# Optimization experiments

Hardware: AMD Instinct MI355X
Metric: run time of the kernel (lower is better)

The kernel has to match this reference:

```python
import itertools
import jax, jax.numpy as jnp
import numpy as np

B, N, C, O = 8, 32, 64, 64
PERMS = list(itertools.permutations((1, 2, 3)))  # build_idx_3_permutations order


def _lin(k, fan_in, out, lead=()):
    # torch nn.Linear default init: U(-1/sqrt(fan_in), 1/sqrt(fan_in)) for W and b
    kw, kb = jax.random.split(k)
    bound = 1.0 / float(np.sqrt(fan_in))
    W = jax.random.uniform(kw, lead + (fan_in, out), minval=-bound, maxval=bound, dtype=jnp.float32)
    b = jax.random.uniform(kb, lead + (out,), minval=-bound, maxval=bound, dtype=jnp.float32)
    return W, b


def setup_inputs() -> dict:
    key = jax.random.key(0)
    ks = jax.random.split(key, 8)
    x = jax.random.normal(ks[0], (B, N, N, N, C), dtype=jnp.float32)
    W33, b33 = _lin(ks[1], 6 * C, O)            # three_to_three linear
    W22, b22 = _lin(ks[2], 12 * C, O, (3,))     # two_to_two (a2 cat transpose), 3 diagonal planes
    W12, b12 = _lin(ks[3], 10 * C, O, (3,))     # one_to_two
    W12t, b12t = _lin(ks[4], 10 * C, O, (3,))   # one_to_two_t
    W02, b02 = _lin(ks[5], 5 * C, O, (3,))      # zero_to_two
    W11, b11 = _lin(ks[6], 10 * C, O)           # one_to_one (in_node_channels = 0)
    W01, b01 = _lin(ks[7], 5 * C, O)            # zero_to_one
    return dict(x=x, W33=W33, b33=b33, W22=W22, b22=b22, W12=W12, b12=b12,
                W12t=W12t, b12t=b12t, W02=W02, b02=b02, W11=W11, b11=b11,
                W01=W01, b01=b01)


def _contractions(x):
    """All second/first/zeroth-order mean contractions of x: [B,n,n,n,C]."""
    s1, s2, s3 = x.mean(1), x.mean(2), x.mean(3)                      # [B,n,n,C]
    # diagonals arranged as [B, other_axis, diag_axis, C]
    d12 = jnp.moveaxis(jnp.diagonal(x, axis1=1, axis2=2), -1, 2)      # [B,n3,diag,C]
    d13 = jnp.moveaxis(jnp.diagonal(x, axis1=1, axis2=3), -1, 2)      # [B,n2,diag,C]
    d23 = jnp.moveaxis(jnp.diagonal(x, axis1=2, axis2=3), -1, 2)      # [B,n1,diag,C]
    a2 = jnp.concatenate([s1, s2, s3, d12, d13, d23], axis=-1)        # [B,n,n,6C]
    tdiag = jnp.moveaxis(jnp.diagonal(d23, axis1=1, axis2=2), -1, 1)  # [B,n,C] triple diagonal x[b,i,i,i]
    a1 = jnp.concatenate([
        x.mean((1, 2)), x.mean((1, 3)), x.mean((2, 3)),               # double sums
        d12.mean(1), d12.mean(2), d13.mean(1), d13.mean(2),           # diag sums
        d23.mean(1), d23.mean(2),
        tdiag], axis=-1)                                              # [B,n,10C]
    a0 = jnp.concatenate([
        x.mean((1, 2, 3)),                                            # triple sum
        d12.mean((1, 2)), d13.mean((1, 2)), d23.mean((1, 2)),         # diag-sum-sum
        tdiag.mean(1)], axis=-1)                                      # [B,5C]
    return a2, a1, a0


def reference(x, W33, b33, W22, b22, W12, b12, W12t, b12t, W02, b02, W11, b11, W01, b01):
    n = x.shape[1]
    a2, a1, a0 = _contractions(x)
    # third-order mix: concat all 6 spatial permutations, then linear 6C -> O
    allp = jnp.concatenate([jnp.transpose(x, (0,) + p + (4,)) for p in PERMS], axis=-1)
    T = allp @ W33 + b33                                              # [B,n,n,n,O]
    # second-order mixes for the 3 diagonal planes
    a2wt = jnp.concatenate([a2, jnp.swapaxes(a2, 1, 2)], axis=-1)     # [B,n,n,12C]
    slices = []
    for i in range(3):
        m = a2wt @ W22[i] + b22[i]
        m = m + (a1 @ W12[i] + b12[i])[:, :, None, :]
        m = m + (a1 @ W12t[i] + b12t[i])[:, None, :, :]
        m = m + (a0 @ W02[i] + b02[i])[:, None, None, :]
        slices.append(m)                                              # [B,n(other),n(diag),O]
    # first-order (core-diagonal) mix
    mdiag = a1 @ W11 + b11 + (a0 @ W01 + b01)[:, None, :]             # [B,n,O]
    # _expand_mix: accumulate slices onto diagonal planes of T (diagonal_free=False)
    idx = jnp.arange(n)
    # plane (1,2): T[b,d,d,t] += slices[0][b,t,d]
    T = T.at[:, idx, idx].add(jnp.swapaxes(slices[0], 1, 2))
    # plane (1,3): T[b,d,t,d] += slices[1][b,t,d]
    Tsw = jnp.swapaxes(T, 2, 3)
    Tsw = Tsw.at[:, idx, idx].add(jnp.swapaxes(slices[1], 1, 2))
    T = jnp.swapaxes(Tsw, 2, 3)
    # plane (2,3): T[b,t,d,d] += slices[2][b,t,d]
    T = T.at[:, :, idx, idx].add(slices[2])
    # triple diagonal: T[b,d,d,d] += mdiag[b,d]
    T = T.at[:, idx, idx, idx].add(mdiag)
    return T
```

## Files before the change

kernel.cpp:

```cpp
#include <hip/hip_runtime.h>

#define NBATCH 8
#define NN 32
#define NC 64
#define NO 64
#define C6 384
#define C10 640
#define C12 768
#define C5 320

typedef __attribute__((ext_vector_type(8))) short short8;
typedef __attribute__((ext_vector_type(4))) float float4v;

static constexpr int OFF_ABF = 0;
static constexpr int OFF_A1  = 1572864;
static constexpr int OFF_A0  = 1736704;
static constexpr int OFF_R1  = 1739264;
static constexpr int OFF_R1T = 1788416;
static constexpr int OFF_R0  = 1837568;
static constexpr int OFF_MD  = 1839104;
static constexpr int OFF_WB  = 1855488;
static constexpr int OFF_WB2 = 1867776;

__device__ __forceinline__ unsigned short f2bf(float f) {
    union { float f; unsigned u; } x{f};
    unsigned r = x.u + 0x7fffu + ((x.u >> 16) & 1u);
    return (unsigned short)(r >> 16);
}

__device__ __forceinline__ void store_bf4(unsigned short* p, float4v v) {
    ushort4 w;
    w.x = f2bf(v.x); w.y = f2bf(v.y); w.z = f2bf(v.z); w.w = f2bf(v.w);
    *(ushort4*)p = w;
}

__device__ __forceinline__ float4v bf4(const unsigned short* p) {
    ushort4 u = *(const ushort4*)(p);
    float4v r;
    r.x = __uint_as_float((unsigned)u.x << 16);
    r.y = __uint_as_float((unsigned)u.y << 16);
    r.z = __uint_as_float((unsigned)u.z << 16);
    r.w = __uint_as_float((unsigned)u.w << 16);
    return r;
}

__global__ __launch_bounds__(256) void k_prepw(const float* __restrict__ W33,
                                               const float* __restrict__ W22,
                                               float* __restrict__ ws) {
    int id = blockIdx.x * 256 + threadIdx.x;
    if (id < 3072) {
        int lane = id & 63;
        int ks = (id >> 6) % 12;
        int nt = (id >> 6) / 12;
        int n = nt * 16 + (lane & 15);
        int k0 = ks * 32 + (lane >> 4) * 8;
        unsigned short* dst = (unsigned short*)(ws + OFF_WB) +
                              (size_t)((nt * 12 + ks) * 64 + lane) * 8;
#pragma unroll
        for (int jj = 0; jj < 8; ++jj) dst[jj] = f2bf(W33[(k0 + jj) * 64 + n]);
    } else if (id < 21504) {
        int q = id - 3072;
        int lane = q & 63;
        int ks = (q >> 6) % 24;
        int r = (q >> 6) / 24;
        int nt = r & 3;
        int i = r >> 2;
        int n = nt * 16 + (lane & 15);
        int k0 = ks * 32 + (lane >> 4) * 8;
        const float* W = W22 + (size_t)i * C12 * NO;
        unsigned short* dst = (unsigned short*)(ws + OFF_WB2) +
                              (size_t)(((i * 4 + nt) * 24 + ks) * 64 + lane) * 8;
#pragma unroll
        for (int jj = 0; jj < 8; ++jj) dst[jj] = f2bf(W[(k0 + jj) * 64 + n]);
    }
}

__global__ __launch_bounds__(256) void k_contract2(const float* __restrict__ x,
                                                   float* __restrict__ ws) {
    int id = blockIdx.x * 256 + threadIdx.x;
    int c4 = id & 15;
    int v = (id >> 4) & 31;
    int u = (id >> 9) & 31;
    int b = id >> 14;
    int bc = c4 * 4;
    const float* xb = x + (size_t)b * 2097152;

    float4v s1 = {0.f, 0.f, 0.f, 0.f}, s2 = s1, s3 = s1;
    {
        const float* p = xb + u * 2048 + v * 64 + bc;
        for (int i = 0; i < 32; ++i) s1 += *(const float4v*)(p + i * 65536);
    }
    {
        const float* p = xb + u * 65536 + v * 64 + bc;
        for (int j = 0; j < 32; ++j) s2 += *(const float4v*)(p + j * 2048);
    }
    {
        const float* p = xb + u * 65536 + v * 2048 + bc;
        for (int k = 0; k < 32; ++k) s3 += *(const float4v*)(p + k * 64);
    }
    float4v d12 = *(const float4v*)(xb + v * 65536 + v * 2048 + u * 64 + bc);
    float4v d13 = *(const float4v*)(xb + v * 65536 + u * 2048 + v * 64 + bc);
    float4v d23 = *(const float4v*)(xb + u * 65536 + v * 2048 + v * 64 + bc);

    const float inv = 1.0f / 32.0f;
    unsigned short* a2 = (unsigned short*)(ws + OFF_ABF) +
                         (size_t)((b * 32 + u) * 32 + v) * C6 + bc;
    store_bf4(a2 + 0 * 64, s1 * inv);
    store_bf4(a2 + 1 * 64, s2 * inv);
    store_bf4(a2 + 2 * 64, s3 * inv);
    store_bf4(a2 + 3 * 64, d12);
    store_bf4(a2 + 4 * 64, d13);
    store_bf4(a2 + 5 * 64, d23);
}

__global__ __launch_bounds__(256) void k_contract1(const float* __restrict__ x,
                                                   float* __restrict__ ws) {
    __shared__ float4v red[16][148];
    int blk = blockIdx.x;
    int b = blk >> 5;
    int t = blk & 31;
    int tid = threadIdx.x;
    int c4 = tid & 15;
    int q = tid >> 4;
    int bc = c4 * 4;
    const unsigned short* a2 = (const unsigned short*)(ws + OFF_ABF) +
                               (size_t)b * 32 * 32 * C6;

    float4v pu0 = {0.f, 0.f, 0.f, 0.f};
    float4v pu3 = pu0, pu4 = pu0, pu5 = pu0;
    float4v pv0 = pu0, pv1 = pu0, pv3 = pu0, pv4 = pu0, pv5 = pu0;
#pragma unroll
    for (int s = 0; s < 2; ++s) {
        int u = q * 2 + s;
        const unsigned short* rU = a2 + (size_t)(u * 32 + t) * C6 + bc;
        const unsigned short* rV = a2 + (size_t)(t * 32 + u) * C6 + bc;
        pu0 += bf4(rU + 0);
        pu3 += bf4(rU + 192);
        pu4 += bf4(rU + 256);
        pu5 += bf4(rU + 320);
        pv0 += bf4(rV + 0);
        pv1 += bf4(rV + 64);
        pv3 += bf4(rV + 192);
        pv4 += bf4(rV + 256);
        pv5 += bf4(rV + 320);
    }
    red[q][0 * 16 + c4] = pu0;
    red[q][1 * 16 + c4] = pv0;
    red[q][2 * 16 + c4] = pv1;
    red[q][3 * 16 + c4] = pu3;
    red[q][4 * 16 + c4] = pv3;
    red[q][5 * 16 + c4] = pu4;
    red[q][6 * 16 + c4] = pv4;
    red[q][7 * 16 + c4] = pu5;
    red[q][8 * 16 + c4] = pv5;
    __syncthreads();

    const float inv = 1.0f / 32.0f;
    float* a1 = ws + OFF_A1 + ((size_t)b * 32 + t) * C10;
    float* a0 = ws + OFF_A0 + (size_t)b * C5;
    if (tid < 144) {
        int ch = tid >> 4;
        int cc = tid & 15;
        float4v s = {0.f, 0.f, 0.f, 0.f};
#pragma unroll
        for (int qq = 0; qq < 16; ++qq) s += red[qq][ch * 16 + cc];
        s *= inv;
        *(float4v*)(a1 + ch * 64 + cc * 4) = s;
        int aidx = (ch == 0) ? 0 : (ch == 3) ? 1 : (ch == 5) ? 2 : (ch == 7) ? 3 : -1;
        if (aidx >= 0) {
#pragma unroll
            for (int e = 0; e < 4; ++e)
                atomicAdd(a0 + aidx * 64 + cc * 4 + e, s[e] * inv);
        }
    } else if (tid < 160) {
        int cc = tid - 144;
        float4v td = *(const float4v*)(x + (((size_t)b * 32 + t) * 32 + t) * 2048 +
                                       t * 64 + cc * 4);
        *(float4v*)(a1 + 9 * 64 + cc * 4) = td;
#pragma unroll
        for (int e = 0; e < 4; ++e)
            atomicAdd(a0 + 4 * 64 + cc * 4 + e, td[e] * inv);
    }
}

__global__ __launch_bounds__(256) void k_rowmix(
    const float* __restrict__ W12, const float* __restrict__ b12,
    const float* __restrict__ W12t, const float* __restrict__ b12t,
    const float* __restrict__ W02, const float* __restrict__ b02,
    const float* __restrict__ W11, const float* __restrict__ b11,
    const float* __restrict__ W01, const float* __restrict__ b01,
    float* __restrict__ ws) {
    int id = blockIdx.x * 256 + threadIdx.x;
    if (id < 98304) {
        bool second = id >= 49152;
        int q = second ? id - 49152 : id;
        int o = q & 63;
        int t = (q >> 6) & 31;
        int b = (q >> 11) & 7;
        int i = q >> 14;
        const float* W = (second ? W12t : W12) + (size_t)i * C10 * NO;
        const float* bb = (second ? b12t : b12) + i * NO;
        const float* a1 = ws + OFF_A1 + ((size_t)b * 32 + t) * C10;
        float acc = bb[o];
        for (int m = 0; m < C10; ++m) acc += a1[m] * W[m * NO + o];
        ws[(second ? OFF_R1T : OFF_R1) + (((size_t)i * 8 + b) * 32 + t) * NO + o] = acc;
    } else if (id < 114688) {
        int q = id - 98304;
        int o = q & 63;
        int t = (q >> 6) & 31;
        int b = q >> 11;
        const float* a1 = ws + OFF_A1 + ((size_t)b * 32 + t) * C10;
        const float* a0 = ws + OFF_A0 + (size_t)b * C5;
        float acc = b11[o] + b01[o];
        for (int m = 0; m < C10; ++m) acc += a1[m] * W11[m * NO + o];
        for (int m = 0; m < C5; ++m) acc += a0[m] * W01[m * NO + o];
        ws[OFF_MD + ((size_t)b * 32 + t) * NO + o] = acc;
    } else if (id < 116224) {
        int q = id - 114688;
        int o = q & 63;
        int b = (q >> 6) & 7;
        int i = q >> 9;
        const float* a0 = ws + OFF_A0 + (size_t)b * C5;
        float acc = b02[i * NO + o];
        for (int m = 0; m < C5; ++m) acc += a0[m] * W02[(size_t)i * C5 * NO + m * NO + o];
        ws[OFF_R0 + ((size_t)i * 8 + b) * NO + o] = acc;
    }
}

__global__ __launch_bounds__(256) void k_main(const float* __restrict__ x,
                                              const float* __restrict__ ws,
                                              const float* __restrict__ b33,
                                              float* __restrict__ T) {
    __shared__ __align__(16) unsigned short As[32 * 392];
    int tid = threadIdx.x;
    const unsigned short* WB = (const unsigned short*)(ws + OFF_WB);

    int wv = tid >> 6;
    int lane = tid & 63;
    int m_tile = wv & 1;
    int n_pair = wv >> 1;
    int colq = lane & 15;
    int quad = lane >> 4;

    short8 bfr[2][12];
#pragma unroll
    for (int np = 0; np < 2; ++np) {
        int nt = n_pair * 2 + np;
#pragma unroll
        for (int ks = 0; ks < 12; ++ks)
            bfr[np][ks] = *(const short8*)(WB + (size_t)((nt * 12 + ks) * 64 + lane) * 8);
    }
    float bb0 = b33[(n_pair * 2 + 0) * 16 + colq];
    float bb1 = b33[(n_pair * 2 + 1) * 16 + colq];

    int k0 = wv * 8;
    int c = colq * 4;
    int mrow = m_tile * 16 + colq;
    const unsigned short* Arow = &As[mrow * 392 + quad * 8];

    int tbase = (blockIdx.x & 7) * 1024 + (blockIdx.x >> 3) * 4;
#pragma unroll 1
    for (int r = 0; r < 4; ++r) {
        int tile = tbase + r;
        int b = tile >> 10;
        int i = (tile >> 5) & 31;
        int j = tile & 31;
        const float* xb = x + (size_t)b * 2097152;

#pragma unroll
        for (int half = 0; half < 2; ++half) {
            int k = k0 + quad + half * 4;
            float4v v0 = *(const float4v*)(xb + i * 65536 + j * 2048 + k * 64 + c);
            float4v v1 = *(const float4v*)(xb + i * 65536 + k * 2048 + j * 64 + c);
            float4v v2 = *(const float4v*)(xb + j * 65536 + i * 2048 + k * 64 + c);
            float4v v3 = *(const float4v*)(xb + k * 65536 + i * 2048 + j * 64 + c);
            float4v v4 = *(const float4v*)(xb + j * 65536 + k * 2048 + i * 64 + c);
            float4v v5 = *(const float4v*)(xb + k * 65536 + j * 2048 + i * 64 + c);
            unsigned short* dst = &As[k * 392 + c];
            store_bf4(dst + 0 * 64, v0);
            store_bf4(dst + 1 * 64, v1);
            store_bf4(dst + 2 * 64, v2);
            store_bf4(dst + 3 * 64, v3);
            store_bf4(dst + 4 * 64, v4);
            store_bf4(dst + 5 * 64, v5);
        }
        __syncthreads();

        float4v acc0 = {0.f, 0.f, 0.f, 0.f};
        float4v acc1 = {0.f, 0.f, 0.f, 0.f};
#pragma unroll
        for (int ks = 0; ks < 12; ++ks) {
            short8 a = *(const short8*)(Arow + ks * 32);
            acc0 = __builtin_amdgcn_mfma_f32_16x16x32_bf16(a, bfr[0][ks], acc0, 0, 0, 0);
            acc1 = __builtin_amdgcn_mfma_f32_16x16x32_bf16(a, bfr[1][ks], acc1, 0, 0, 0);
        }

        float* Tb = T + (size_t)tile * 2048;
#pragma unroll
        for (int rr = 0; rr < 4; ++rr) {
            int m = m_tile * 16 + quad * 4 + rr;
            int o0 = (n_pair * 2 + 0) * 16 + colq;
            int o1 = (n_pair * 2 + 1) * 16 + colq;
            __builtin_nontemporal_store(acc0[rr] + bb0, &Tb[m * 64 + o0]);
            __builtin_nontemporal_store(acc1[rr] + bb1, &Tb[m * 64 + o1]);
        }
        __syncthreads();
    }
}

__global__ __launch_bounds__(512) void k_slices(const float* __restrict__ b22,
                                                float* __restrict__ T,
                                                const float* __restrict__ ws) {
    __shared__ __align__(16) unsigned short As[32 * 776];
    int blk = blockIdx.x;
    int b = blk >> 5;
    int t = blk & 31;
    int tid = threadIdx.x;
    const unsigned short* abf = (const unsigned short*)(ws + OFF_ABF);
    const unsigned short* WB2 = (const unsigned short*)(ws + OFF_WB2);

    for (int l = tid; l < 3072; l += 512) {
        int d = l / 96;
        int m8 = l - d * 96;
        const unsigned short* src = (m8 < 48)
            ? abf + (size_t)(((b * 32 + t) * 32 + d) * C6) + m8 * 8
            : abf + (size_t)(((b * 32 + d) * 32 + t) * C6) + (m8 - 48) * 8;
        *(short8*)&As[d * 776 + m8 * 8] = *(const short8*)src;
    }
    __syncthreads();

    int wv = tid >> 6;
    int lane = tid & 63;
    int mt = wv & 1;
    int nt = wv >> 1;
    float4v zero = {0.f, 0.f, 0.f, 0.f};
    float4v acc[3] = {zero, zero, zero};
    const unsigned short* Arow = &As[(mt * 16 + (lane & 15)) * 776 + (lane >> 4) * 8];
#pragma unroll
    for (int ks = 0; ks < 24; ++ks) {
        short8 a = *(const short8*)(Arow + ks * 32);
#pragma unroll
        for (int i = 0; i < 3; ++i) {
            short8 bf = *(const short8*)(WB2 + (size_t)(((i * 4 + nt) * 24 + ks) * 64 + lane) * 8);
            acc[i] = __builtin_amdgcn_mfma_f32_16x16x32_bf16(a, bf, acc[i], 0, 0, 0);
        }
    }

    int colq = lane & 15;
    int quad = lane >> 4;
    float* Tb = T + (size_t)b * 2097152;
    int o = nt * 16 + colq;
    float base0 = b22[0 * 64 + o] + ws[OFF_R1 + ((size_t)(0 * 8 + b) * 32 + t) * 64 + o]
                + ws[OFF_R0 + (size_t)(0 * 8 + b) * 64 + o];
    float base1 = b22[1 * 64 + o] + ws[OFF_R1 + ((size_t)(1 * 8 + b) * 32 + t) * 64 + o]
                + ws[OFF_R0 + (size_t)(1 * 8 + b) * 64 + o];
    float base2 = b22[2 * 64 + o] + ws[OFF_R1 + ((size_t)(2 * 8 + b) * 32 + t) * 64 + o]
                + ws[OFF_R0 + (size_t)(2 * 8 + b) * 64 + o];
#pragma unroll
    for (int r = 0; r < 4; ++r) {
        int d = mt * 16 + quad * 4 + r;
        float s0 = acc[0][r] + base0 + ws[OFF_R1T + ((size_t)(0 * 8 + b) * 32 + d) * 64 + o];
        float s1 = acc[1][r] + base1 + ws[OFF_R1T + ((size_t)(1 * 8 + b) * 32 + d) * 64 + o];
        float s2 = acc[2][r] + base2 + ws[OFF_R1T + ((size_t)(2 * 8 + b) * 32 + d) * 64 + o];
        if (d != t) {
            Tb[d * 65536 + d * 2048 + t * 64 + o] += s0;
            Tb[d * 65536 + t * 2048 + d * 64 + o] += s1;
            Tb[t * 65536 + d * 2048 + d * 64 + o] += s2;
        } else {
            float md = ws[OFF_MD + ((size_t)b * 32 + d) * 64 + o];
            Tb[d * 65536 + d * 2048 + d * 64 + o] += s0 + s1 + s2 + md;
        }
    }
}

extern "C" void kernel_launch(void* const* d_in, const int* in_sizes, int n_in,
                              void* d_out, int out_size, void* d_ws, size_t ws_size,
                              hipStream_t stream) {
    const float* x    = (const float*)d_in[0];
    const float* W33  = (const float*)d_in[1];
    const float* b33  = (const float*)d_in[2];
    const float* W22  = (const float*)d_in[3];
    const float* b22  = (const float*)d_in[4];
    const float* W12  = (const float*)d_in[5];
    const float* b12  = (const float*)d_in[6];
    const float* W12t = (const float*)d_in[7];
    const float* b12t = (const float*)d_in[8];
    const float* W02  = (const float*)d_in[9];
    const float* b02  = (const float*)d_in[10];
    const float* W11  = (const float*)d_in[11];
    const float* b11  = (const float*)d_in[12];
    const float* W01  = (const float*)d_in[13];
    const float* b01  = (const float*)d_in[14];
    float* T  = (float*)d_out;
    float* ws = (float*)d_ws;

    hipLaunchKernelGGL(k_prepw, dim3(84), dim3(256), 0, stream, W33, W22, ws);
    hipLaunchKernelGGL(k_contract2, dim3(512), dim3(256), 0, stream, x, ws);
    hipMemsetAsync(ws + OFF_A0, 0, (size_t)NBATCH * C5 * sizeof(float), stream);
    hipLaunchKernelGGL(k_contract1, dim3(256), dim3(256), 0, stream, x, ws);
    hipLaunchKernelGGL(k_rowmix, dim3(454), dim3(256), 0, stream,
                       W12, b12, W12t, b12t, W02, b02, W11, b11, W01, b01, ws);
    hipLaunchKernelGGL(k_main, dim3(2048), dim3(256), 0, stream, x, ws, b33, T);
    hipLaunchKernelGGL(k_slices, dim3(256), dim3(512), 0, stream, b22, T, ws);
}
```

Baseline: 250.4 us.

## Fuse weight prep with contraction and fold row mixes into neighbouring kernels

Merges the weight bf16 repacking kernel with the second-order contraction kernel into one launch, computes the W12/W12t row mixes inside k_contract1 from a shared-memory copy of a1, and computes the diagonal and zeroth-order mixes inside k_slices. This removes two kernel launches and the separate k_rowmix pass with its global round trips. In exchange, k_contract1 and k_slices each do extra serial dot-product work per block, which could lengthen their critical path.

New measurement: 274.4 us. +9.6%, slower.

```diff
diff --git a/kernel.cpp b/kernel.cpp
--- a/kernel.cpp
+++ b/kernel.cpp
@@ -44,40 +44,40 @@
     return r;
 }
 
-__global__ __launch_bounds__(256) void k_prepw(const float* __restrict__ W33,
+__global__ __launch_bounds__(256) void k_prep2(const float* __restrict__ W33,
                                                const float* __restrict__ W22,
+                                               const float* __restrict__ x,
                                                float* __restrict__ ws) {
-    int id = blockIdx.x * 256 + threadIdx.x;
-    if (id < 3072) {
-        int lane = id & 63;
-        int ks = (id >> 6) % 12;
-        int nt = (id >> 6) / 12;
-        int n = nt * 16 + (lane & 15);
-        int k0 = ks * 32 + (lane >> 4) * 8;
-        unsigned short* dst = (unsigned short*)(ws + OFF_WB) +
-                              (size_t)((nt * 12 + ks) * 64 + lane) * 8;
-#pragma unroll
-        for (int jj = 0; jj < 8; ++jj) dst[jj] = f2bf(W33[(k0 + jj) * 64 + n]);
-    } else if (id < 21504) {
-        int q = id - 3072;
-        int lane = q & 63;
-        int ks = (q >> 6) % 24;
-        int r = (q >> 6) / 24;
-        int nt = r & 3;
-        int i = r >> 2;
-        int n = nt * 16 + (lane & 15);
-        int k0 = ks * 32 + (lane >> 4) * 8;
-        const float* W = W22 + (size_t)i * C12 * NO;
-        unsigned short* dst = (unsigned short*)(ws + OFF_WB2) +
-                              (size_t)(((i * 4 + nt) * 24 + ks) * 64 + lane) * 8;
-#pragma unroll
-        for (int jj = 0; jj < 8; ++jj) dst[jj] = f2bf(W[(k0 + jj) * 64 + n]);
-    }
-}
-
-__global__ __launch_bounds__(256) void k_contract2(const float* __restrict__ x,
-                                                   float* __restrict__ ws) {
-    int id = blockIdx.x * 256 + threadIdx.x;
+    if (blockIdx.x < 84) {
+        int id = blockIdx.x * 256 + threadIdx.x;
+        if (id < 3072) {
+            int lane = id & 63;
+            int ks = (id >> 6) % 12;
+            int nt = (id >> 6) / 12;
+            int n = nt * 16 + (lane & 15);
+            int k0 = ks * 32 + (lane >> 4) * 8;
+            unsigned short* dst = (unsigned short*)(ws + OFF_WB) +
+                                  (size_t)((nt * 12 + ks) * 64 + lane) * 8;
+#pragma unroll
+            for (int jj = 0; jj < 8; ++jj) dst[jj] = f2bf(W33[(k0 + jj) * 64 + n]);
+        } else if (id < 21504) {
+            int q = id - 3072;
+            int lane = q & 63;
+            int ks = (q >> 6) % 24;
+            int r = (q >> 6) / 24;
+            int nt = r & 3;
+            int i = r >> 2;
+            int n = nt * 16 + (lane & 15);
+            int k0 = ks * 32 + (lane >> 4) * 8;
+            const float* W = W22 + (size_t)i * C12 * NO;
+            unsigned short* dst = (unsigned short*)(ws + OFF_WB2) +
+                                  (size_t)(((i * 4 + nt) * 24 + ks) * 64 + lane) * 8;
+#pragma unroll
+            for (int jj = 0; jj < 8; ++jj) dst[jj] = f2bf(W[(k0 + jj) * 64 + n]);
+        }
+        return;
+    }
+    int id = (blockIdx.x - 84) * 256 + threadIdx.x;
     int c4 = id & 15;
     int v = (id >> 4) & 31;
     int u = (id >> 9) & 31;
@@ -113,9 +113,13 @@
     store_bf4(a2 + 5 * 64, d23);
 }
 
-__global__ __launch_bounds__(256) void k_contract1(const float* __restrict__ x,
-                                                   float* __restrict__ ws) {
+__global__ __launch_bounds__(256) void k_contract1(
+    const float* __restrict__ x,
+    const float* __restrict__ W12, const float* __restrict__ b12,
+    const float* __restrict__ W12t, const float* __restrict__ b12t,
+    float* __restrict__ ws) {
     __shared__ float4v red[16][148];
+    __shared__ float a1buf[C10];
     int blk = blockIdx.x;
     int b = blk >> 5;
     int t = blk & 31;
@@ -166,6 +170,8 @@
         for (int qq = 0; qq < 16; ++qq) s += red[qq][ch * 16 + cc];
         s *= inv;
         *(float4v*)(a1 + ch * 64 + cc * 4) = s;
+#pragma unroll
+        for (int e = 0; e < 4; ++e) a1buf[ch * 64 + cc * 4 + e] = s[e];
         int aidx = (ch == 0) ? 0 : (ch == 3) ? 1 : (ch == 5) ? 2 : (ch == 7) ? 3 : -1;
         if (aidx >= 0) {
 #pragma unroll
@@ -178,52 +184,32 @@
                                        t * 64 + cc * 4);
         *(float4v*)(a1 + 9 * 64 + cc * 4) = td;
 #pragma unroll
-        for (int e = 0; e < 4; ++e)
+        for (int e = 0; e < 4; ++e) {
+            a1buf[9 * 64 + cc * 4 + e] = td[e];
             atomicAdd(a0 + 4 * 64 + cc * 4 + e, td[e] * inv);
-    }
-}
-
-__global__ __launch_bounds__(256) void k_rowmix(
-    const float* __restrict__ W12, const float* __restrict__ b12,
-    const float* __restrict__ W12t, const float* __restrict__ b12t,
-    const float* __restrict__ W02, const float* __restrict__ b02,
-    const float* __restrict__ W11, const float* __restrict__ b11,
-    const float* __restrict__ W01, const float* __restrict__ b01,
-    float* __restrict__ ws) {
-    int id = blockIdx.x * 256 + threadIdx.x;
-    if (id < 98304) {
-        bool second = id >= 49152;
-        int q = second ? id - 49152 : id;
-        int o = q & 63;
-        int t = (q >> 6) & 31;
-        int b = (q >> 11) & 7;
-        int i = q >> 14;
-        const float* W = (second ? W12t : W12) + (size_t)i * C10 * NO;
-        const float* bb = (second ? b12t : b12) + i * NO;
-        const float* a1 = ws + OFF_A1 + ((size_t)b * 32 + t) * C10;
-        float acc = bb[o];
-        for (int m = 0; m < C10; ++m) acc += a1[m] * W[m * NO + o];
-        ws[(second ? OFF_R1T : OFF_R1) + (((size_t)i * 8 + b) * 32 + t) * NO + o] = acc;
-    } else if (id < 114688) {
-        int q = id - 98304;
-        int o = q & 63;
-        int t = (q >> 6) & 31;
-        int b = q >> 11;
-        const float* a1 = ws + OFF_A1 + ((size_t)b * 32 + t) * C10;
-        const float* a0 = ws + OFF_A0 + (size_t)b * C5;
-        float acc = b11[o] + b01[o];
-        for (int m = 0; m < C10; ++m) acc += a1[m] * W11[m * NO + o];
-        for (int m = 0; m < C5; ++m) acc += a0[m] * W01[m * NO + o];
-        ws[OFF_MD + ((size_t)b * 32 + t) * NO + o] = acc;
-    } else if (id < 116224) {
-        int q = id - 114688;
-        int o = q & 63;
-        int b = (q >> 6) & 7;
-        int i = q >> 9;
-        const float* a0 = ws + OFF_A0 + (size_t)b * C5;
-        float acc = b02[i * NO + o];
-        for (int m = 0; m < C5; ++m) acc += a0[m] * W02[(size_t)i * C5 * NO + m * NO + o];
-        ws[OFF_R0 + ((size_t)i * 8 + b) * NO + o] = acc;
+        }
+    }
+    __syncthreads();
+
+    for (int out = tid; out < 384; out += 256) {
+        int v = out >> 6;
+        int o = out & 63;
+        const float* W;
+        float acc;
+        if (v < 3) { W = W12  + (size_t)v * C10 * NO;       acc = b12[v * NO + o]; }
+        else       { W = W12t + (size_t)(v - 3) * C10 * NO; acc = b12t[(v - 3) * NO + o]; }
+        float m0 = 0.f, m1 = 0.f, m2 = 0.f, m3 = 0.f;
+        for (int m = 0; m < C10; m += 4) {
+            m0 += a1buf[m + 0] * W[(m + 0) * NO + o];
+            m1 += a1buf[m + 1] * W[(m + 1) * NO + o];
+            m2 += a1buf[m + 2] * W[(m + 2) * NO + o];
+            m3 += a1buf[m + 3] * W[(m + 3) * NO + o];
+        }
+        acc += (m0 + m1) + (m2 + m3);
+        size_t idx = (v < 3)
+            ? OFF_R1  + (((size_t)v * 8 + b) * 32 + t) * NO + o
+            : OFF_R1T + (((size_t)(v - 3) * 8 + b) * 32 + t) * NO + o;
+        ws[idx] = acc;
     }
 }
 
@@ -308,10 +294,15 @@
     }
 }
 
-__global__ __launch_bounds__(512) void k_slices(const float* __restrict__ b22,
-                                                float* __restrict__ T,
-                                                const float* __restrict__ ws) {
+__global__ __launch_bounds__(512) void k_slices(
+    const float* __restrict__ b22,
+    const float* __restrict__ W11, const float* __restrict__ b11,
+    const float* __restrict__ W01, const float* __restrict__ b01,
+    const float* __restrict__ W02, const float* __restrict__ b02,
+    float* __restrict__ T, const float* __restrict__ ws) {
     __shared__ __align__(16) unsigned short As[32 * 776];
+    __shared__ float md[64];
+    __shared__ float r0s[3][64];
     int blk = blockIdx.x;
     int b = blk >> 5;
     int t = blk & 31;
@@ -327,6 +318,39 @@
             : abf + (size_t)(((b * 32 + d) * 32 + t) * C6) + (m8 - 48) * 8;
         *(short8*)&As[d * 776 + m8 * 8] = *(const short8*)src;
     }
+
+    if (tid < 64) {
+        int o = tid;
+        const float* a1g = ws + OFF_A1 + ((size_t)b * 32 + t) * C10;
+        const float* a0g = ws + OFF_A0 + (size_t)b * C5;
+        float m0 = 0.f, m1 = 0.f, m2 = 0.f, m3 = 0.f;
+        for (int m = 0; m < C10; m += 4) {
+            m0 += a1g[m + 0] * W11[(m + 0) * NO + o];
+            m1 += a1g[m + 1] * W11[(m + 1) * NO + o];
+            m2 += a1g[m + 2] * W11[(m + 2) * NO + o];
+            m3 += a1g[m + 3] * W11[(m + 3) * NO + o];
+        }
+        for (int m = 0; m < C5; m += 4) {
+            m0 += a0g[m + 0] * W01[(m + 0) * NO + o];
+            m1 += a0g[m + 1] * W01[(m + 1) * NO + o];
+            m2 += a0g[m + 2] * W01[(m + 2) * NO + o];
+            m3 += a0g[m + 3] * W01[(m + 3) * NO + o];
+        }
+        md[o] = b11[o] + b01[o] + (m0 + m1) + (m2 + m3);
+    } else if (tid < 256) {
+        int i = (tid - 64) >> 6;
+        int o = tid & 63;
+        const float* a0g = ws + OFF_A0 + (size_t)b * C5;
+        const float* W = W02 + (size_t)i * C5 * NO;
+        float m0 = 0.f, m1 = 0.f, m2 = 0.f, m3 = 0.f;
+        for (int m = 0; m < C5; m += 4) {
+            m0 += a0g[m + 0] * W[(m + 0) * NO + o];
+            m1 += a0g[m + 1] * W[(m + 1) * NO + o];
+            m2 += a0g[m + 2] * W[(m + 2) * NO + o];
+            m3 += a0g[m + 3] * W[(m + 3) * NO + o];
+        }
+        r0s[i][o] = b02[i * NO + o] + (m0 + m1) + (m2 + m3);
+    }
     __syncthreads();
 
     int wv = tid >> 6;
@@ -351,11 +375,11 @@
     float* Tb = T + (size_t)b * 2097152;
     int o = nt * 16 + colq;
     float base0 = b22[0 * 64 + o] + ws[OFF_R1 + ((size_t)(0 * 8 + b) * 32 + t) * 64 + o]
-                + ws[OFF_R0 + (size_t)(0 * 8 + b) * 64 + o];
+                + r0s[0][o];
     float base1 = b22[1 * 64 + o] + ws[OFF_R1 + ((size_t)(1 * 8 + b) * 32 + t) * 64 + o]
-                + ws[OFF_R0 + (size_t)(1 * 8 + b) * 64 + o];
+                + r0s[1][o];
     float base2 = b22[2 * 64 + o] + ws[OFF_R1 + ((size_t)(2 * 8 + b) * 32 + t) * 64 + o]
-                + ws[OFF_R0 + (size_t)(2 * 8 + b) * 64 + o];
+                + r0s[2][o];
 #pragma unroll
     for (int r = 0; r < 4; ++r) {
         int d = mt * 16 + quad * 4 + r;
@@ -367,8 +391,7 @@
             Tb[d * 65536 + t * 2048 + d * 64 + o] += s1;
             Tb[t * 65536 + d * 2048 + d * 64 + o] += s2;
         } else {
-            float md = ws[OFF_MD + ((size_t)b * 32 + d) * 64 + o];
-            Tb[d * 65536 + d * 2048 + d * 64 + o] += s0 + s1 + s2 + md;
+            Tb[d * 65536 + d * 2048 + d * 64 + o] += s0 + s1 + s2 + md[o];
         }
     }
 }
@@ -394,12 +417,11 @@
     float* T  = (float*)d_out;
     float* ws = (float*)d_ws;
 
-    hipLaunchKernelGGL(k_prepw, dim3(84), dim3(256), 0, stream, W33, W22, ws);
-    hipLaunchKernelGGL(k_contract2, dim3(512), dim3(256), 0, stream, x, ws);
     hipMemsetAsync(ws + OFF_A0, 0, (size_t)NBATCH * C5 * sizeof(float), stream);
-    hipLaunchKernelGGL(k_contract1, dim3(256), dim3(256), 0, stream, x, ws);
-    hipLaunchKernelGGL(k_rowmix, dim3(454), dim3(256), 0, stream,
-                       W12, b12, W12t, b12t, W02, b02, W11, b11, W01, b01, ws);
+    hipLaunchKernelGGL(k_prep2, dim3(596), dim3(256), 0, stream, W33, W22, x, ws);
+    hipLaunchKernelGGL(k_contract1, dim3(256), dim3(256), 0, stream,
+                       x, W12, b12, W12t, b12t, ws);
     hipLaunchKernelGGL(k_main, dim3(2048), dim3(256), 0, stream, x, ws, b33, T);
-    hipLaunchKernelGGL(k_slices, dim3(256), dim3(512), 0, stream, b22, T, ws);
-}
+    hipLaunchKernelGGL(k_slices, dim3(256), dim3(512), 0, stream,
+                       b22, W11, b11, W01, b01, W02, b02, T, ws);
+}
```
